# Performance work log

Measured on AMD Instinct MI355X. Metric: run time of the kernel, lower is better.

Reference implementation:

```python
import jax, jax.numpy as jnp
import numpy as np

B, L, H, E = 4, 2048, 8, 64
NEG = -1e30  # stand-in for the repo's -3.4e38 overflow-to-inf masking trick


def setup_inputs() -> dict:
    key = jax.random.key(0)
    kq, kk, kv = jax.random.split(key, 3)
    return {
        "queries": jax.random.normal(kq, (B, L, H, E), dtype=jnp.float32),
        "keys": jax.random.normal(kk, (B, L, H, E), dtype=jnp.float32),
        "values": jax.random.normal(kv, (B, L, H, E), dtype=jnp.float32),
    }


def reference(queries, keys, values):
    b, l, h, e = queries.shape
    s = keys.shape[1]
    scale = 1.0 / np.sqrt(e).astype(np.float32)
    # [B,H,L,S] scores, materialized as in the original einsum
    scores = jnp.einsum('blhe,bshe->bhls', queries, keys)
    causal = jnp.tril(jnp.ones((l, s), dtype=bool))  # True = visible
    scores = jnp.where(causal, scores, NEG)
    A = jax.nn.softmax(scale * scores, axis=-1)  # dropout is identity at inference
    return jnp.einsum('bhls,bshd->blhd', A, values)
```

## Files before the change

kernel.cpp:

```cpp
#include <hip/hip_runtime.h>
#include <hip/hip_bf16.h>

namespace {

constexpr int B_ = 4, L = 2048, H = 8, E = 64;
constexpr int RS = H * E;
constexpr float CS = 0.125f * 1.44269504f;
constexpr float THR2 = 11.5f;

constexpr size_t ACCF = (size_t)2 * 32 * 8 * 128 * 64;
constexpr size_t MOFF = ACCF;
constexpr size_t PART_ROWS = (size_t)32 * 8 * 128;
constexpr size_t LOFF = MOFF + 2 * PART_ROWS;
constexpr size_t WS_FLOATS = LOFF + 2 * PART_ROWS;

typedef __attribute__((ext_vector_type(8))) short bf16x8;
typedef __attribute__((ext_vector_type(4))) float f32x4;

__device__ inline unsigned cvt2(float a, float b) {
  __hip_bfloat162 hh = __float22bfloat162_rn(make_float2(a, b));
  union { __hip_bfloat162 h; unsigned u; } c; c.h = hh; return c.u;
}

__global__ __launch_bounds__(512)
void fa_split(const float* __restrict__ Q, const float* __restrict__ K,
              const float* __restrict__ V, float* __restrict__ O,
              float* __restrict__ ws, int splitMode)
{
  const int tid  = (int)threadIdx.x;
  const int lane = tid & 63;
  const int wv   = tid >> 6;
  const int bi   = (int)blockIdx.x;
  const int bh   = bi & 31;
  const int pp   = (bi >> 5) & 7;
  const int role = splitMode ? (bi >> 8) : 2;
  const int b = bh >> 3, h = bh & 7;
  const int ln = lane & 15, lg = lane >> 4, d0 = lg * 4;

  int total, ph1sb0, qgA, k0A, qgB; bool finA, finB; int part;
  const int g = pp, v = 15 - pp;
  if (role == 0)      { total = 17; ph1sb0 = 2*g+2; qgA = g; k0A = 0;        finA = true;  qgB = v; finB = false; part = 0; }
  else if (role == 1) { total = 17; ph1sb0 = 1000;  qgA = v; k0A = 15 - 2*g; finA = false; qgB = 0; finB = false; part = 1; }
  else                { total = 34; ph1sb0 = 2*g+2; qgA = g; k0A = 0;        finA = true;  qgB = v; finB = true;  part = 0; }

  const size_t base = (size_t)b * L * RS + (size_t)h * E;
  const float* Qb = Q + base;
  const float* Kb = K + base;
  const float* Vb = V + base;
  float*       Ob = O + base;

  __shared__ __align__(16) unsigned char KT[2][64 * 128];
  __shared__ __align__(16) unsigned char VT[2][64 * 128];

  const int vdd = tid & 63, vkq = tid >> 6;
  const int kky = tid >> 3, kc  = tid & 7;
  float vr[8]; float4 kr0, kr1;

  auto stage_load = [&](int ks) {
    const int kv0 = ks * 64;
    const float* vp = Vb + (size_t)(kv0 + 8 * vkq) * RS + vdd;
#pragma unroll
    for (int j = 0; j < 8; ++j) vr[j] = vp[(size_t)j * RS];
    const float* kp = Kb + (size_t)(kv0 + kky) * RS + 8 * kc;
    kr0 = *(const float4*)kp; kr1 = *(const float4*)(kp + 4);
  };
  auto stage_write = [&](int bufI) {
    union { uint4 q; unsigned u[4]; } w;
    w.u[0] = cvt2(vr[0], vr[1]); w.u[1] = cvt2(vr[2], vr[3]);
    w.u[2] = cvt2(vr[4], vr[5]); w.u[3] = cvt2(vr[6], vr[7]);
    *(uint4*)(VT[bufI] + vdd * 128 + 16 * (vkq ^ (vdd & 7))) = w.q;
    union { uint4 q; unsigned u[4]; } y;
    y.u[0] = cvt2(kr0.x, kr0.y); y.u[1] = cvt2(kr0.z, kr0.w);
    y.u[2] = cvt2(kr1.x, kr1.y); y.u[3] = cvt2(kr1.z, kr1.w);
    *(uint4*)(KT[bufI] + kky * 128 + 16 * (kc ^ (kky & 7))) = y.q;
  };

  int qg = qgA; bool curFin = finA;
  int qrow0 = qg * 128 + wv * 16;
  int nsW   = (qrow0 + 79) >> 6;

  bf16x8 qf0, qf1;
  auto load_q = [&]() {
    const float* qp = Qb + (size_t)(qrow0 + ln) * RS + 8 * lg;
    float4 a = *(const float4*)qp,        c = *(const float4*)(qp + 4);
    float4 d = *(const float4*)(qp + 32), e = *(const float4*)(qp + 36);
    union { bf16x8 v8; unsigned u[4]; } r0, r1;
    r0.u[0] = cvt2(a.x * CS, a.y * CS); r0.u[1] = cvt2(a.z * CS, a.w * CS);
    r0.u[2] = cvt2(c.x * CS, c.y * CS); r0.u[3] = cvt2(c.z * CS, c.w * CS);
    r1.u[0] = cvt2(d.x * CS, d.y * CS); r1.u[1] = cvt2(d.z * CS, d.w * CS);
    r1.u[2] = cvt2(e.x * CS, e.y * CS); r1.u[3] = cvt2(e.z * CS, e.w * CS);
    qf0 = r0.v8; qf1 = r1.v8;
  };
  load_q();

  f32x4 acc[4];
#pragma unroll
  for (int nt = 0; nt < 4; ++nt) acc[nt] = (f32x4){0.f, 0.f, 0.f, 0.f};
  float m = -1e30f, lsum = 0.f;

  auto epilogue = [&]() {
    if (curFin) {
      const float il = 1.0f / lsum;
      float inv[4];
#pragma unroll
      for (int r = 0; r < 4; ++r) inv[r] = __shfl(il, d0 + r, 64);
#pragma unroll
      for (int nt = 0; nt < 4; ++nt)
#pragma unroll
        for (int r = 0; r < 4; ++r)
          Ob[(size_t)(qrow0 + d0 + r) * RS + (ln + 16 * nt)] = acc[nt][r] * inv[r];
    } else {
      const int vg = qg - 8;
      const size_t rb = ((size_t)part * 32 + bh) * 1024 + (size_t)vg * 128;
#pragma unroll
      for (int nt = 0; nt < 4; ++nt)
#pragma unroll
        for (int r = 0; r < 4; ++r)
          ws[(rb + wv * 16 + d0 + r) * 64 + ln + 16 * nt] = acc[nt][r];
      if (lane < 16) {
        ws[MOFF + rb + wv * 16 + lane] = m;
        ws[LOFF + rb + wv * 16 + lane] = lsum;
      }
    }
  };

  stage_load(k0A);
  stage_write(0);
  __syncthreads();
  int buf = 0;

  for (int sb = 0; sb < total; ++sb) {
    const bool haveNext = (sb + 1) < total;
    if (haveNext) {
      const int sn = sb + 1;
      stage_load((sn < ph1sb0) ? (k0A + sn) : (sn - ph1sb0));
    }
    const int kstep = (sb < ph1sb0) ? (k0A + sb) : (sb - ph1sb0);

    if (kstep < nsW) {
      const unsigned char* Kt = KT[buf];
      const int swzr = 16 * (ln & 7);

      f32x4 st[4];
#pragma unroll
      for (int kt = 0; kt < 4; ++kt) {
        const unsigned char* kr = Kt + (16 * kt + ln) * 128;
        const bf16x8 kfa = *(const bf16x8*)(kr + ((16 * lg) ^ swzr));
        const bf16x8 kfb = *(const bf16x8*)(kr + ((16 * lg + 64) ^ swzr));
        f32x4 s = (f32x4){0.f, 0.f, 0.f, 0.f};
        s = __builtin_amdgcn_mfma_f32_16x16x32_bf16(kfa, qf0, s, 0, 0, 0);
        s = __builtin_amdgcn_mfma_f32_16x16x32_bf16(kfb, qf1, s, 0, 0, 0);
        st[kt] = s;
      }

      float x[16];
#pragma unroll
      for (int kt = 0; kt < 4; ++kt)
#pragma unroll
        for (int r = 0; r < 4; ++r) x[4 * kt + r] = st[kt][r];

      if (kstep == nsW - 1) {
        const int kv0 = kstep * 64;
        const int qr = qrow0 + ln;
#pragma unroll
        for (int kt = 0; kt < 4; ++kt)
#pragma unroll
          for (int r = 0; r < 4; ++r) {
            const int key = kv0 + 16 * kt + d0 + r;
            if (key > qr) x[4 * kt + r] = -1e30f;
          }
      }

      float mx = x[0];
#pragma unroll
      for (int e = 1; e < 16; ++e) mx = fmaxf(mx, x[e]);
      mx = fmaxf(mx, __shfl_xor(mx, 16, 64));
      mx = fmaxf(mx, __shfl_xor(mx, 32, 64));

      if (!__all(mx <= m + THR2)) {
        const float newm = fmaxf(m, mx);
        const float sc = __builtin_exp2f(m - newm);
        lsum *= sc;
        float scr[4];
#pragma unroll
        for (int r = 0; r < 4; ++r) scr[r] = __shfl(sc, d0 + r, 64);
#pragma unroll
        for (int nt = 0; nt < 4; ++nt) {
          acc[nt][0] *= scr[0]; acc[nt][1] *= scr[1];
          acc[nt][2] *= scr[2]; acc[nt][3] *= scr[3];
        }
        m = newm;
      }

      float p[16]; float ps = 0.f;
#pragma unroll
      for (int e = 0; e < 16; ++e) { p[e] = __builtin_exp2f(x[e] - m); ps += p[e]; }
      ps += __shfl_xor(ps, 16, 64);
      ps += __shfl_xor(ps, 32, 64);
      lsum += ps;

      const unsigned char* Vt = VT[buf];
#pragma unroll
      for (int kg = 0; kg < 2; ++kg) {
        union { bf16x8 v8; unsigned u[4]; } pf;
#pragma unroll
        for (int j = 0; j < 4; ++j)
          pf.u[j] = cvt2(p[8 * kg + 2 * j], p[8 * kg + 2 * j + 1]);
#pragma unroll
        for (int nt = 0; nt < 4; ++nt) {
          const int row = ln + 16 * nt;
          const unsigned char* vrow = Vt + row * 128;
          const int sz = 16 * (row & 7);
          union { bf16x8 v8; uint2 p2[2]; } vf;
          vf.p2[0] = *(const uint2*)(vrow + ((8 * lg + 64 * kg) ^ sz));
          vf.p2[1] = *(const uint2*)(vrow + ((8 * lg + 32 + 64 * kg) ^ sz));
          acc[nt] = __builtin_amdgcn_mfma_f32_16x16x32_bf16(pf.v8, vf.v8, acc[nt], 0, 0, 0);
        }
      }
    }

    if (sb == ph1sb0 - 1) {
      epilogue();
#pragma unroll
      for (int nt = 0; nt < 4; ++nt) acc[nt] = (f32x4){0.f, 0.f, 0.f, 0.f};
      m = -1e30f; lsum = 0.f;
      qg = qgB; curFin = finB;
      qrow0 = qg * 128 + wv * 16;
      nsW = (qrow0 + 79) >> 6;
      load_q();
    }

    if (haveNext) stage_write(buf ^ 1);
    __syncthreads();
    buf ^= 1;
  }

  epilogue();
}

__global__ __launch_bounds__(256)
void fa_merge(const float* __restrict__ ws, float* __restrict__ O)
{
  const int idx = (int)blockIdx.x * 256 + (int)threadIdx.x;
  const int d4  = idx & 15;
  const int row = (idx >> 4) & 127;
  const int vg  = (idx >> 11) & 7;
  const int bh  = idx >> 14;
  const size_t rbase = ((size_t)bh * 8 + vg) * 128 + row;

  const float m0 = ws[MOFF + rbase],             l0 = ws[LOFF + rbase];
  const float m1 = ws[MOFF + PART_ROWS + rbase], l1 = ws[LOFF + PART_ROWS + rbase];
  const float M  = fmaxf(m0, m1);
  const float e0 = __builtin_exp2f(m0 - M), e1 = __builtin_exp2f(m1 - M);
  const float inv = 1.0f / (l0 * e0 + l1 * e1);

  const float4 a0 = *(const float4*)(ws + rbase * 64 + 4 * d4);
  const float4 a1 = *(const float4*)(ws + PART_ROWS * 64 + rbase * 64 + 4 * d4);

  const int b = bh >> 3, h = bh & 7;
  const int orow = (8 + vg) * 128 + row;
  float4 o;
  o.x = (a0.x * e0 + a1.x * e1) * inv;
  o.y = (a0.y * e0 + a1.y * e1) * inv;
  o.z = (a0.z * e0 + a1.z * e1) * inv;
  o.w = (a0.w * e0 + a1.w * e1) * inv;
  *(float4*)(O + ((size_t)(b * L + orow) * H + h) * E + 4 * d4) = o;
}

}

extern "C" void kernel_launch(void* const* d_in, const int* in_sizes, int n_in,
                              void* d_out, int out_size, void* d_ws, size_t ws_size,
                              hipStream_t stream) {
  const float* Q = (const float*)d_in[0];
  const float* K = (const float*)d_in[1];
  const float* V = (const float*)d_in[2];
  float* O = (float*)d_out;
  (void)in_sizes; (void)n_in; (void)out_size;

  const bool split = ws_size >= WS_FLOATS * sizeof(float);
  if (split) {
    fa_split<<<512, 512, 0, stream>>>(Q, K, V, O, (float*)d_ws, 1);
    fa_merge<<<2048, 256, 0, stream>>>((const float*)d_ws, O);
  } else {
    fa_split<<<256, 512, 0, stream>>>(Q, K, V, O, (float*)d_ws, 0);
  }
}
```

Before: 56.85 us.

## Pre-pack K/V into swizzled bf16 tiles and stream them via global_load_lds

Adds a repack kernel that converts K and V to bf16 once per call and stores them as pre-swizzled 8KB tiles in the workspace. The attention kernel then fills its LDS tiles directly with global_load_lds DMA instead of loading fp32 into registers, converting and writing to LDS. This is meant to remove redundant fp32 reads, conversions and LDS-store work from the main loop and cut register pressure. The cost is an extra launch and an extra pass over K/V, and it only runs when the workspace is large enough.

```diff
diff --git a/kernel.cpp b/kernel.cpp
--- a/kernel.cpp
+++ b/kernel.cpp
@@ -8,11 +8,16 @@
 constexpr float CS = 0.125f * 1.44269504f;
 constexpr float THR2 = 11.5f;
 
+constexpr size_t TILE_BYTES = 8192;
+constexpr size_t NTILES = 32 * 32;
+constexpr size_t KIMG_BYTES = NTILES * TILE_BYTES;
+constexpr size_t IMG_FLOATS = 2 * KIMG_BYTES / 4;
+
 constexpr size_t ACCF = (size_t)2 * 32 * 8 * 128 * 64;
 constexpr size_t MOFF = ACCF;
 constexpr size_t PART_ROWS = (size_t)32 * 8 * 128;
 constexpr size_t LOFF = MOFF + 2 * PART_ROWS;
-constexpr size_t WS_FLOATS = LOFF + 2 * PART_ROWS;
+constexpr size_t PART_FLOATS = LOFF + 2 * PART_ROWS;
 
 typedef __attribute__((ext_vector_type(8))) short bf16x8;
 typedef __attribute__((ext_vector_type(4))) float f32x4;
@@ -22,9 +27,50 @@
   union { __hip_bfloat162 h; unsigned u; } c; c.h = hh; return c.u;
 }
 
+__global__ __launch_bounds__(256)
+void repack(const float* __restrict__ K, const float* __restrict__ V,
+            unsigned char* __restrict__ img)
+{
+  const int tid = (int)threadIdx.x;
+  const int bi  = (int)blockIdx.x;
+  const int bh  = bi & 31, t = bi >> 5;
+  const int b = bh >> 3, h = bh & 7;
+  const size_t base = (size_t)b * L * RS + (size_t)h * E;
+  const int kv0 = t * 64;
+  const int row = tid >> 2, c0 = (tid & 3) * 2;
+
+  unsigned char* Kimg = img + (size_t)(bh * 32 + t) * TILE_BYTES;
+  unsigned char* Vimg = img + KIMG_BYTES + (size_t)(bh * 32 + t) * TILE_BYTES;
+
+  {
+    const float4* kp = (const float4*)(K + base + (size_t)(kv0 + row) * RS + 8 * c0);
+    const float4 a = kp[0], bq = kp[1], c = kp[2], d = kp[3];
+    uint4 w0; w0.x = cvt2(a.x, a.y);  w0.y = cvt2(a.z, a.w);
+              w0.z = cvt2(bq.x, bq.y); w0.w = cvt2(bq.z, bq.w);
+    uint4 w1; w1.x = cvt2(c.x, c.y);  w1.y = cvt2(c.z, c.w);
+              w1.z = cvt2(d.x, d.y);  w1.w = cvt2(d.z, d.w);
+    *(uint4*)(Kimg + row * 128 + 16 * (c0 ^ (row & 7)))       = w0;
+    *(uint4*)(Kimg + row * 128 + 16 * ((c0 + 1) ^ (row & 7))) = w1;
+  }
+  {
+    const float* vp = V + base + (size_t)(kv0 + 8 * c0) * RS + row;
+    float v[16];
+#pragma unroll
+    for (int j = 0; j < 16; ++j) v[j] = vp[(size_t)j * RS];
+    uint4 w0; w0.x = cvt2(v[0], v[1]);   w0.y = cvt2(v[2], v[3]);
+              w0.z = cvt2(v[4], v[5]);   w0.w = cvt2(v[6], v[7]);
+    uint4 w1; w1.x = cvt2(v[8], v[9]);   w1.y = cvt2(v[10], v[11]);
+              w1.z = cvt2(v[12], v[13]); w1.w = cvt2(v[14], v[15]);
+    *(uint4*)(Vimg + row * 128 + 16 * (c0 ^ (row & 7)))       = w0;
+    *(uint4*)(Vimg + row * 128 + 16 * ((c0 + 1) ^ (row & 7))) = w1;
+  }
+}
+
+template<bool PACKED>
 __global__ __launch_bounds__(512)
 void fa_split(const float* __restrict__ Q, const float* __restrict__ K,
               const float* __restrict__ V, float* __restrict__ O,
+              const unsigned char* __restrict__ img,
               float* __restrict__ ws, int splitMode)
 {
   const int tid  = (int)threadIdx.x;
@@ -52,6 +98,17 @@
   __shared__ __align__(16) unsigned char KT[2][64 * 128];
   __shared__ __align__(16) unsigned char VT[2][64 * 128];
 
+  auto stage_issue = [&](int ks, int bufI) {
+    const unsigned char* kg = img + (size_t)(bh * 32 + ks) * TILE_BYTES + tid * 16;
+    const unsigned char* vg = img + KIMG_BYTES + (size_t)(bh * 32 + ks) * TILE_BYTES + tid * 16;
+    __builtin_amdgcn_global_load_lds(
+        (const __attribute__((address_space(1))) void*)kg,
+        (__attribute__((address_space(3))) void*)(&KT[bufI][tid * 16]), 16, 0, 0);
+    __builtin_amdgcn_global_load_lds(
+        (const __attribute__((address_space(1))) void*)vg,
+        (__attribute__((address_space(3))) void*)(&VT[bufI][tid * 16]), 16, 0, 0);
+  };
+
   const int vdd = tid & 63, vkq = tid >> 6;
   const int kky = tid >> 3, kc  = tid & 7;
   float vr[8]; float4 kr0, kr1;
@@ -124,8 +181,12 @@
     }
   };
 
-  stage_load(k0A);
-  stage_write(0);
+  if constexpr (PACKED) {
+    stage_issue(k0A, 0);
+  } else {
+    stage_load(k0A);
+    stage_write(0);
+  }
   __syncthreads();
   int buf = 0;
 
@@ -133,7 +194,9 @@
     const bool haveNext = (sb + 1) < total;
     if (haveNext) {
       const int sn = sb + 1;
-      stage_load((sn < ph1sb0) ? (k0A + sn) : (sn - ph1sb0));
+      const int nks = (sn < ph1sb0) ? (k0A + sn) : (sn - ph1sb0);
+      if constexpr (PACKED) stage_issue(nks, buf ^ 1);
+      else                  stage_load(nks);
     }
     const int kstep = (sb < ph1sb0) ? (k0A + sb) : (sb - ph1sb0);
 
@@ -230,7 +293,7 @@
       load_q();
     }
 
-    if (haveNext) stage_write(buf ^ 1);
+    if constexpr (!PACKED) { if (haveNext) stage_write(buf ^ 1); }
     __syncthreads();
     buf ^= 1;
   }
@@ -278,11 +341,17 @@
   float* O = (float*)d_out;
   (void)in_sizes; (void)n_in; (void)out_size;
 
-  const bool split = ws_size >= WS_FLOATS * sizeof(float);
-  if (split) {
-    fa_split<<<512, 512, 0, stream>>>(Q, K, V, O, (float*)d_ws, 1);
+  const bool full = ws_size >= (IMG_FLOATS + PART_FLOATS) * sizeof(float);
+  const bool mid  = ws_size >= PART_FLOATS * sizeof(float);
+  if (full) {
+    repack<<<1024, 256, 0, stream>>>(K, V, (unsigned char*)d_ws);
+    float* parts = (float*)d_ws + IMG_FLOATS;
+    fa_split<true><<<512, 512, 0, stream>>>(Q, K, V, O, (const unsigned char*)d_ws, parts, 1);
+    fa_merge<<<2048, 256, 0, stream>>>(parts, O);
+  } else if (mid) {
+    fa_split<false><<<512, 512, 0, stream>>>(Q, K, V, O, nullptr, (float*)d_ws, 1);
     fa_merge<<<2048, 256, 0, stream>>>((const float*)d_ws, O);
   } else {
-    fa_split<<<256, 512, 0, stream>>>(Q, K, V, O, (float*)d_ws, 0);
-  }
-}
+    fa_split<false><<<256, 512, 0, stream>>>(Q, K, V, O, nullptr, (float*)d_ws, 0);
+  }
+}
```

Measured after the change: 64.46 us. 1.13x slower.
